# Performance work log

Measured on AMD Instinct MI355X. Metric: run time of the kernel, lower is better.

Reference implementation:

```python
import jax, jax.numpy as jnp
import numpy as np

B, C, H, W = 4, 128, 64, 64

def _conv1x1(x, w, b):
    # 1x1 conv == per-pixel GEMM: [B,C,H,W] x [O,C] -> [B,O,H,W]
    return jnp.einsum('bchw,oc->bohw', x, w) + b[None, :, None, None]

def setup_inputs() -> dict:
    key = jax.random.key(0)
    ks = jax.random.split(key, 11)
    s = 0.02
    return {
        'x0': jax.random.normal(ks[0], (B, C, H, W), jnp.float32),
        'x1': jax.random.normal(ks[1], (B, C, H, W), jnp.float32),
        'g_w': jax.random.normal(ks[2], (C, C), jnp.float32) * s,
        'g_b': jax.random.normal(ks[3], (C,), jnp.float32) * s,
        'theta_w': jax.random.normal(ks[4], (C, C), jnp.float32) * s,
        'theta_b': jax.random.normal(ks[5], (C,), jnp.float32) * s,
        'phi_w': jax.random.normal(ks[6], (C, C), jnp.float32) * s,
        'phi_b': jax.random.normal(ks[7], (C,), jnp.float32) * s,
        'W_w': jax.random.normal(ks[8], (C, C), jnp.float32) * s,
        'W_b': jax.random.normal(ks[9], (C,), jnp.float32) * s,
    }

def reference(x0, x1, g_w, g_b, theta_w, theta_b, phi_w, phi_b, W_w, W_b):
    b, c, h, w = x0.shape
    # g, phi from x0; theta from x1 (cross-attention style)
    g_x = _conv1x1(x0, g_w, g_b).reshape(b, c, -1)          # [B,C,N]
    theta_x = _conv1x1(x1, theta_w, theta_b).reshape(b, c, -1)  # [B,C,N]
    phi_x = _conv1x1(x0, phi_w, phi_b).reshape(b, c, -1)    # [B,C,N]
    # unscaled single-head attention over N=H*W spatial positions
    f = jnp.einsum('bcn,bcm->bnm', theta_x, phi_x)          # [B,N,N]
    attn = jax.nn.softmax(f, axis=-1)
    y = jnp.einsum('bnm,bcm->bcn', attn, g_x)               # [B,C,N]
    y = y.reshape(b, c, h, w)
    return _conv1x1(y, W_w, W_b)
```

## Files before the change

### kernel.cpp

```cpp
#include <hip/hip_runtime.h>
#include <hip/hip_bf16.h>
#include <stdint.h>

#define BB 4
#define CC 128
#define NN 4096
#define NSEG 6
#define KVBLK 32

#define LOG2E 1.4426950408889634f

typedef __bf16 bf16_t;
typedef bf16_t bf16x8 __attribute__((ext_vector_type(8)));
typedef float f32x4 __attribute__((ext_vector_type(4)));
typedef float f32x16 __attribute__((ext_vector_type(16)));
typedef int v2i __attribute__((ext_vector_type(2)));
typedef unsigned int u32;
typedef unsigned short u16;

#if __has_builtin(__builtin_amdgcn_exp2f)
#define EXP2(x) __builtin_amdgcn_exp2f(x)
#else
#define EXP2(x) exp2f(x)
#endif

__device__ __forceinline__ u16 f2bf(float f) {
  union { float f; u32 u; } v; v.f = f;
  u32 r = v.u + 0x7FFFu + ((v.u >> 16) & 1u);
  return (u16)(r >> 16);
}
__device__ __forceinline__ float bf2f(u16 x) {
  union { u32 u; float f; } v; v.u = ((u32)x) << 16; return v.f;
}

__device__ __forceinline__ bf16x8 ldfrag(const u16* p) {
  return *reinterpret_cast<const bf16x8*>(p);
}

__device__ __forceinline__ f32x4 mfma16(bf16x8 a, bf16x8 b, f32x4 c) {
  return __builtin_amdgcn_mfma_f32_16x16x32_bf16(a, b, c, 0, 0, 0);
}
__device__ __forceinline__ f32x16 mfma32(bf16x8 a, bf16x8 b, f32x16 c) {
  return __builtin_amdgcn_mfma_f32_32x32x16_bf16(a, b, c, 0, 0, 0);
}
__device__ __forceinline__ u32 cvtpk(float lo, float hi) {
  u32 d; asm("v_cvt_pk_bf16_f32 %0, %1, %2" : "=v"(d) : "v"(lo), "v"(hi)); return d;
}

__device__ __forceinline__ void async_cp16(const void* g, void* l) {
  __builtin_amdgcn_global_load_lds(
      (const __attribute__((address_space(1))) void*)g,
      (__attribute__((address_space(3))) void*)l, 16, 0, 0);
}

__global__ __launch_bounds__(256) void proj_kernel(
    const float* __restrict__ x0, const float* __restrict__ x1,
    const float* __restrict__ g_w, const float* __restrict__ g_b,
    const float* __restrict__ th_w, const float* __restrict__ th_b,
    const float* __restrict__ ph_w, const float* __restrict__ ph_b,
    u16* __restrict__ qws, u16* __restrict__ kws, u16* __restrict__ vws)
{
  const int t = threadIdx.x;
  const int nt0 = blockIdx.x * 64;
  const int b = blockIdx.y;
  const int p = blockIdx.z;

  __shared__ __align__(16) u16 W_lds[128][136];
  __shared__ __align__(16) u16 xT_lds[64][136];

  const float* x    = (p == 0) ? x1 : x0;
  const float* w    = (p == 0) ? th_w : (p == 1) ? ph_w : g_w;
  const float* bias = (p == 0) ? th_b : (p == 1) ? ph_b : g_b;

  for (int i = 0; i < 16; ++i) {
    int s = t + i * 256;
    int row = s >> 5, c4 = s & 31;
    float4 v = *reinterpret_cast<const float4*>(w + row * 128 + c4 * 4);
    u32 lo = (u32)f2bf(v.x) | ((u32)f2bf(v.y) << 16);
    u32 hi = (u32)f2bf(v.z) | ((u32)f2bf(v.w) << 16);
    *reinterpret_cast<uint2*>(&W_lds[row][c4 * 4]) = make_uint2(lo, hi);
  }
  for (int i = 0; i < 8; ++i) {
    int s = t + i * 256;
    int cp = s >> 4;
    int nc = s & 15;
    float4 v = *reinterpret_cast<const float4*>(x + ((size_t)b * CC + cp) * NN + nt0 + nc * 4);
    xT_lds[nc * 4 + 0][cp] = f2bf(v.x);
    xT_lds[nc * 4 + 1][cp] = f2bf(v.y);
    xT_lds[nc * 4 + 2][cp] = f2bf(v.z);
    xT_lds[nc * 4 + 3][cp] = f2bf(v.w);
  }
  __syncthreads();

  const int w_id = t >> 6, l = t & 63;
  const int lr = l & 15, lh = l >> 4;

  if (p < 2) {
    const float osc = (p == 0) ? LOG2E : 1.0f;
    f32x4 acc[8];
#pragma unroll
    for (int ct = 0; ct < 8; ++ct) acc[ct] = (f32x4){0.f, 0.f, 0.f, 0.f};
#pragma unroll
    for (int kc = 0; kc < 4; ++kc) {
      bf16x8 a = ldfrag(&xT_lds[w_id * 16 + lr][kc * 32 + lh * 8]);
#pragma unroll
      for (int ct = 0; ct < 8; ++ct) {
        bf16x8 bf = ldfrag(&W_lds[ct * 16 + lr][kc * 32 + lh * 8]);
        acc[ct] = mfma16(a, bf, acc[ct]);
      }
    }
    u16* outp = (p == 0) ? qws : kws;
#pragma unroll
    for (int ct = 0; ct < 8; ++ct) {
      float bv = bias[ct * 16 + lr];
#pragma unroll
      for (int r = 0; r < 4; ++r) {
        int n = nt0 + w_id * 16 + lh * 4 + r;
        outp[((size_t)b * NN + n) * CC + ct * 16 + lr] = f2bf((acc[ct][r] + bv) * osc);
      }
    }
  } else {
    f32x4 acc[2][4];
#pragma unroll
    for (int rt = 0; rt < 2; ++rt)
#pragma unroll
      for (int nt = 0; nt < 4; ++nt) acc[rt][nt] = (f32x4){0.f, 0.f, 0.f, 0.f};
#pragma unroll
    for (int kc = 0; kc < 4; ++kc) {
      bf16x8 a0 = ldfrag(&W_lds[w_id * 32 + lr][kc * 32 + lh * 8]);
      bf16x8 a1 = ldfrag(&W_lds[w_id * 32 + 16 + lr][kc * 32 + lh * 8]);
#pragma unroll
      for (int nt = 0; nt < 4; ++nt) {
        bf16x8 bf = ldfrag(&xT_lds[nt * 16 + lr][kc * 32 + lh * 8]);
        acc[0][nt] = mfma16(a0, bf, acc[0][nt]);
        acc[1][nt] = mfma16(a1, bf, acc[1][nt]);
      }
    }
#pragma unroll
    for (int rt = 0; rt < 2; ++rt)
#pragma unroll
      for (int r = 0; r < 4; ++r) {
        int c = w_id * 32 + rt * 16 + lh * 4 + r;
        float bv = bias[c];
#pragma unroll
        for (int nt = 0; nt < 4; ++nt) {
          vws[((size_t)b * CC + c) * NN + nt0 + nt * 16 + lr] = f2bf(acc[rt][nt][r] + bv);
        }
      }
  }
}

__global__ __launch_bounds__(256, 3) void attn_kernel(
    const u16* __restrict__ qws, const u16* __restrict__ kws,
    const u16* __restrict__ vws, u16* __restrict__ yacc,
    float* __restrict__ ml)
{
  const int t = threadIdx.x, wv = t >> 6, l = t & 63;
  const int l31 = l & 31, hi = l >> 5;
  const int q0 = blockIdx.x * 128;
  const int b = blockIdx.y, seg = blockIdx.z;
  const int grp = b * NSEG + seg;
  const int ch0 = (seg < 2) ? seg * 22 : 44 + (seg - 2) * 21;
  const int nch = (seg < 2) ? 22 : 21;
  const int m_base = ch0 * KVBLK;

  __shared__ __align__(16) u16 smem[4 * 4096];
  char* sb = (char*)smem;

  bf16x8 qf[8];
  {
    const u16* qp = qws + ((size_t)b * NN + q0 + wv * 32 + l31) * CC + hi * 8;
#pragma unroll
    for (int kc = 0; kc < 8; ++kc) qf[kc] = *reinterpret_cast<const bf16x8*>(qp + kc * 16);
  }

  const u32 koff = ((u32)(l & 31)) * 256 + ((u32)(wv * 2 + (l >> 5))) * 16;
  const u32 voff = ((u32)((wv & 1) * 64 + l)) * 8192 + ((u32)(wv >> 1)) * 16;
  const char* kgb = (const char*)(kws + ((size_t)b * NN + m_base) * CC);
  const char* vgb = (const char*)(vws + (size_t)b * CC * NN) + (size_t)m_base * 2;

#define ISSUE_K(CH, BOFF) do {                                                       \
    async_cp16(kgb + (size_t)(CH) * 8192 + koff,       sb + (BOFF) + wv * 1024);     \
    async_cp16(kgb + (size_t)(CH) * 8192 + koff + 128, sb + (BOFF) + wv * 1024 + 4096); \
  } while (0)
#define ISSUE_V(CH, BOFF) do {                                                       \
    async_cp16(vgb + (size_t)(CH) * 64 + voff,      sb + (BOFF) + wv * 1024);        \
    async_cp16(vgb + (size_t)(CH) * 64 + voff + 32, sb + (BOFF) + wv * 1024 + 4096); \
  } while (0)
#define SCHED0() __builtin_amdgcn_sched_barrier(0)
#define BAR() do { SCHED0(); __builtin_amdgcn_s_barrier(); SCHED0(); } while (0)

  f32x16 yt[4];
#pragma unroll
  for (int ct = 0; ct < 4; ++ct)
#pragma unroll
    for (int r = 0; r < 16; ++r) yt[ct][r] = 0.f;
  float l_run = 0.f;
  f32x16 stA, stB;
  bf16x8 pbA, pbB;

#define QK_BLOCK(KBASE) do {                                                     \
    const u16* kb = (const u16*)(sb + (KBASE)) + hi * 256 + l31 * 8;             \
    _Pragma("unroll")                                                            \
    for (int r = 0; r < 16; ++r) { stA[r] = 0.f; stB[r] = 0.f; }                 \
    _Pragma("unroll")                                                            \
    for (int kc = 0; kc < 4; ++kc) {                                             \
      stA = mfma32(ldfrag(kb + kc * 512),       qf[kc],     stA);                \
      stB = mfma32(ldfrag(kb + (kc + 4) * 512), qf[kc + 4], stB);                \
    }                                                                            \
  } while (0)

#define PV_BLOCK(VBASE) do {                                                     \
    const u16* vb = (const u16*)(sb + (VBASE)) + hi * 1024 + l31 * 8;            \
    _Pragma("unroll")                                                            \
    for (int ct = 0; ct < 4; ++ct)                                               \
      yt[ct] = mfma32(ldfrag(vb + ct * 256), pbA, yt[ct]);                       \
    _Pragma("unroll")                                                            \
    for (int ct = 0; ct < 4; ++ct)                                               \
      yt[ct] = mfma32(ldfrag(vb + 2048 + ct * 256), pbB, yt[ct]);                \
  } while (0)

#define PACK8(SS, OFF, DEST) do {                                                \
    u32 X0 = cvtpk(SS[(OFF) + 0], SS[(OFF) + 1]);                                \
    u32 X1 = cvtpk(SS[(OFF) + 2], SS[(OFF) + 3]);                                \
    u32 X4 = cvtpk(SS[(OFF) + 4], SS[(OFF) + 5]);                                \
    u32 X5 = cvtpk(SS[(OFF) + 6], SS[(OFF) + 7]);                                \
    v2i s1 = __builtin_amdgcn_permlane32_swap((int)X0, (int)X4, false, false);   \
    v2i s2 = __builtin_amdgcn_permlane32_swap((int)X1, (int)X5, false, false);   \
    int4 bw = make_int4(s1.x, s2.x, s1.y, s2.y);                                 \
    DEST = *reinterpret_cast<bf16x8*>(&bw);                                      \
  } while (0)

#define SM_CONVERT() do {                                                        \
    _Pragma("unroll")                                                            \
    for (int r = 0; r < 16; ++r) stA[r] = EXP2(stA[r] + stB[r]);                 \
    PACK8(stA, 0, pbA);                                                          \
    PACK8(stA, 8, pbB);                                                          \
    _Pragma("unroll")                                                            \
    for (int i2 = 0; i2 < 8; ++i2) stA[i2] = stA[i2] + stA[i2 + 8];              \
    _Pragma("unroll")                                                            \
    for (int i2 = 0; i2 < 4; ++i2) stA[i2] = stA[i2] + stA[i2 + 4];              \
    float ps = (stA[0] + stA[1]) + (stA[2] + stA[3]);                            \
    ps += __shfl_xor(ps, 32);                                                    \
    l_run += ps;                                                                 \
  } while (0)

  ISSUE_K(0, 0);
  ISSUE_K(1, 8192);
  ISSUE_V(0, 16384);
  asm volatile("s_waitcnt vmcnt(4)" ::: "memory");
  BAR();
  QK_BLOCK(0);
  SM_CONVERT();
  asm volatile("s_waitcnt vmcnt(0)" ::: "memory");
  BAR();
  ISSUE_K(2, 0);
  ISSUE_V(1, 24576);

  for (int ch = 1; ch < nch; ++ch) {
    const u32 bK  = (u32)(ch & 1) * 8192;
    const u32 bVp = 16384 + (u32)((ch - 1) & 1) * 8192;
    __builtin_amdgcn_s_setprio(1);
    QK_BLOCK(bK);
    PV_BLOCK(bVp);
    __builtin_amdgcn_s_setprio(0);
    SM_CONVERT();
    asm volatile("s_waitcnt vmcnt(0)" ::: "memory");
    BAR();
    if (ch + 2 < nch) ISSUE_K(ch + 2, bK);
    if (ch + 1 < nch) ISSUE_V(ch + 1, bVp);
  }
  __builtin_amdgcn_s_setprio(1);
  PV_BLOCK(16384 + (u32)((nch - 1) & 1) * 8192);
  __builtin_amdgcn_s_setprio(0);

#undef QK_BLOCK
#undef PV_BLOCK
#undef PACK8
#undef SM_CONVERT
#undef ISSUE_K
#undef ISSUE_V

  __syncthreads();
  const float inv_l = 1.0f / l_run;
  if (l < 32) {
    const size_t row_g = (size_t)grp * NN + q0 + wv * 32 + l31;
    ml[row_g] = l_run;
  }
  u16* yp_base = yacc + ((size_t)grp * NN + q0 + wv * 32) * CC;
#pragma unroll
  for (int half = 0; half < 2; ++half) {
    if ((wv >> 1) == half) {
      u16* eps = smem + (wv & 1) * 4352;
#pragma unroll
      for (int ct = 0; ct < 4; ++ct)
#pragma unroll
        for (int g = 0; g < 4; ++g) {
          u32 w0 = cvtpk(yt[ct][4 * g + 0] * inv_l, yt[ct][4 * g + 1] * inv_l);
          u32 w1 = cvtpk(yt[ct][4 * g + 2] * inv_l, yt[ct][4 * g + 3] * inv_l);
          *reinterpret_cast<uint2*>(&eps[l31 * 136 + ct * 32 + g * 8 + hi * 4]) = make_uint2(w0, w1);
        }
#pragma unroll
      for (int pass = 0; pass < 8; ++pass) {
        int q_r = pass * 4 + (l >> 4);
        int cchunk = (l & 15) * 8;
        uint4 v = *reinterpret_cast<const uint4*>(&eps[q_r * 136 + cchunk]);
        *reinterpret_cast<uint4*>(yp_base + (size_t)q_r * CC + cchunk) = v;
      }
    }
    __syncthreads();
  }
}

__global__ __launch_bounds__(256) void outproj_kernel(
    const u16* __restrict__ yacc, const float* __restrict__ ml,
    const float* __restrict__ Ww, const float* __restrict__ Wb,
    float* __restrict__ out)
{
  const int t = threadIdx.x;
  const int nt0 = blockIdx.x * 64;
  const int b = blockIdx.y;

  __shared__ __align__(16) u16 W_lds[128][136];
  __shared__ __align__(16) u16 y_lds[64][136];

  for (int i = 0; i < 16; ++i) {
    int s = t + i * 256;
    int row = s >> 5, c4 = s & 31;
    float4 v = *reinterpret_cast<const float4*>(Ww + row * 128 + c4 * 4);
    u32 lo = (u32)f2bf(v.x) | ((u32)f2bf(v.y) << 16);
    u32 hi = (u32)f2bf(v.z) | ((u32)f2bf(v.w) << 16);
    *reinterpret_cast<uint2*>(&W_lds[row][c4 * 4]) = make_uint2(lo, hi);
  }
#pragma unroll
  for (int pass = 0; pass < 4; ++pass) {
    int row = pass * 16 + (t >> 4);
    int li = t & 15;
    int n = nt0 + row;
    float l_s[NSEG];
    float Wsum = 0.f;
#pragma unroll
    for (int s = 0; s < NSEG; ++s) {
      l_s[s] = ml[(size_t)(b * NSEG + s) * NN + n];
      Wsum += l_s[s];
    }
    float inv = 1.0f / Wsum;
    float o[8];
#pragma unroll
    for (int j = 0; j < 8; ++j) o[j] = 0.f;
#pragma unroll
    for (int s = 0; s < NSEG; ++s) {
      uint4 v = *reinterpret_cast<const uint4*>(
          yacc + ((size_t)(b * NSEG + s) * NN + n) * CC + li * 8);
      const u16* h = reinterpret_cast<const u16*>(&v);
      float w = l_s[s];
#pragma unroll
      for (int j = 0; j < 8; ++j) o[j] += w * bf2f(h[j]);
    }
    u32 p0 = (u32)f2bf(o[0] * inv) | ((u32)f2bf(o[1] * inv) << 16);
    u32 p1 = (u32)f2bf(o[2] * inv) | ((u32)f2bf(o[3] * inv) << 16);
    u32 p2 = (u32)f2bf(o[4] * inv) | ((u32)f2bf(o[5] * inv) << 16);
    u32 p3 = (u32)f2bf(o[6] * inv) | ((u32)f2bf(o[7] * inv) << 16);
    *reinterpret_cast<uint4*>(&y_lds[row][li * 8]) = make_uint4(p0, p1, p2, p3);
  }
  __syncthreads();

  const int w_id = t >> 6, l = t & 63;
  const int lr = l & 15, lh = l >> 4;

  f32x4 acc[2][4];
#pragma unroll
  for (int rt = 0; rt < 2; ++rt)
#pragma unroll
    for (int nt = 0; nt < 4; ++nt) acc[rt][nt] = (f32x4){0.f, 0.f, 0.f, 0.f};
#pragma unroll
  for (int kc = 0; kc < 4; ++kc) {
    bf16x8 a0 = ldfrag(&W_lds[w_id * 32 + lr][kc * 32 + lh * 8]);
    bf16x8 a1 = ldfrag(&W_lds[w_id * 32 + 16 + lr][kc * 32 + lh * 8]);
#pragma unroll
    for (int nt = 0; nt < 4; ++nt) {
      bf16x8 bf = ldfrag(&y_lds[nt * 16 + lr][kc * 32 + lh * 8]);
      acc[0][nt] = mfma16(a0, bf, acc[0][nt]);
      acc[1][nt] = mfma16(a1, bf, acc[1][nt]);
    }
  }
#pragma unroll
  for (int rt = 0; rt < 2; ++rt)
#pragma unroll
    for (int r = 0; r < 4; ++r) {
      int c = w_id * 32 + rt * 16 + lh * 4 + r;
      float bv = Wb[c];
#pragma unroll
      for (int nt = 0; nt < 4; ++nt)
        out[((size_t)b * CC + c) * NN + nt0 + nt * 16 + lr] = acc[rt][nt][r] + bv;
    }
}

extern "C" void kernel_launch(void* const* d_in, const int* in_sizes, int n_in,
                              void* d_out, int out_size, void* d_ws, size_t ws_size,
                              hipStream_t stream) {
  const float* x0   = (const float*)d_in[0];
  const float* x1   = (const float*)d_in[1];
  const float* g_w  = (const float*)d_in[2];
  const float* g_b  = (const float*)d_in[3];
  const float* th_w = (const float*)d_in[4];
  const float* th_b = (const float*)d_in[5];
  const float* ph_w = (const float*)d_in[6];
  const float* ph_b = (const float*)d_in[7];
  const float* Ww   = (const float*)d_in[8];
  const float* Wb   = (const float*)d_in[9];

  char* ws = (char*)d_ws;
  u16* qws    = (u16*)(ws + 0);
  u16* kws    = (u16*)(ws + (size_t)4194304);
  u16* vws    = (u16*)(ws + (size_t)8388608);
  float* mlp  = (float*)(ws + (size_t)12582912);
  u16* yacc   = (u16*)(ws + (size_t)13631488);

  dim3 gp(64, 4, 3);
  proj_kernel<<<gp, 256, 0, stream>>>(x0, x1, g_w, g_b, th_w, th_b, ph_w, ph_b,
                                      qws, kws, vws);
  dim3 ga(32, 4, NSEG);
  attn_kernel<<<ga, 256, 0, stream>>>(qws, kws, vws, yacc, mlp);
  dim3 go(64, 4);
  outproj_kernel<<<go, 256, 0, stream>>>(yacc, mlp, Ww, Wb, (float*)d_out);
}
```

Before: 65.27 us.

## Retile attention to 16x16 MFMA with 64-query blocks and four KV segments

The attention kernel moves from 32x32x16 MFMA tiles over 32 queries per wave to 16x16x32 MFMA tiles over 16 queries per wave, so each block now covers 64 queries. The probability tile is staged through a small per-wave LDS buffer instead of being rearranged with permlane swaps. The KV split drops from six uneven segments to four equal ones, the grid grows along the query axis, and the occupancy hint rises to 4 blocks per CU. The goal is more, lighter blocks and fewer partial results to merge, at the cost of reloading each K/V tile for fewer queries and using the smaller MFMA shape.

```diff
diff --git a/kernel.cpp b/kernel.cpp
--- a/kernel.cpp
+++ b/kernel.cpp
@@ -5,16 +5,17 @@
 #define BB 4
 #define CC 128
 #define NN 4096
-#define NSEG 6
+#define NSEG 4
+#define SEGLEN (NN / NSEG)
 #define KVBLK 32
+#define NCH (SEGLEN / KVBLK)
 
 #define LOG2E 1.4426950408889634f
+#define PPITCH 40
 
 typedef __bf16 bf16_t;
 typedef bf16_t bf16x8 __attribute__((ext_vector_type(8)));
 typedef float f32x4 __attribute__((ext_vector_type(4)));
-typedef float f32x16 __attribute__((ext_vector_type(16)));
-typedef int v2i __attribute__((ext_vector_type(2)));
 typedef unsigned int u32;
 typedef unsigned short u16;
 
@@ -39,9 +40,6 @@
 
 __device__ __forceinline__ f32x4 mfma16(bf16x8 a, bf16x8 b, f32x4 c) {
   return __builtin_amdgcn_mfma_f32_16x16x32_bf16(a, b, c, 0, 0, 0);
-}
-__device__ __forceinline__ f32x16 mfma32(bf16x8 a, bf16x8 b, f32x16 c) {
-  return __builtin_amdgcn_mfma_f32_32x32x16_bf16(a, b, c, 0, 0, 0);
 }
 __device__ __forceinline__ u32 cvtpk(float lo, float hi) {
   u32 d; asm("v_cvt_pk_bf16_f32 %0, %1, %2" : "=v"(d) : "v"(lo), "v"(hi)); return d;
@@ -150,28 +148,27 @@
   }
 }
 
-__global__ __launch_bounds__(256, 3) void attn_kernel(
+__global__ __launch_bounds__(256, 4) void attn_kernel(
     const u16* __restrict__ qws, const u16* __restrict__ kws,
     const u16* __restrict__ vws, u16* __restrict__ yacc,
     float* __restrict__ ml)
 {
   const int t = threadIdx.x, wv = t >> 6, l = t & 63;
-  const int l31 = l & 31, hi = l >> 5;
-  const int q0 = blockIdx.x * 128;
+  const int q16 = l & 15, g = l >> 4;
+  const int q0 = blockIdx.x * 64;
   const int b = blockIdx.y, seg = blockIdx.z;
   const int grp = b * NSEG + seg;
-  const int ch0 = (seg < 2) ? seg * 22 : 44 + (seg - 2) * 21;
-  const int nch = (seg < 2) ? 22 : 21;
-  const int m_base = ch0 * KVBLK;
-
-  __shared__ __align__(16) u16 smem[4 * 4096];
+  const int m_base = seg * SEGLEN;
+
+  __shared__ __align__(16) u16 smem[16384 + 4 * 16 * PPITCH];
   char* sb = (char*)smem;
-
-  bf16x8 qf[8];
+  u16* Pw = smem + 16384 + wv * (16 * PPITCH);
+
+  bf16x8 qf[4];
   {
-    const u16* qp = qws + ((size_t)b * NN + q0 + wv * 32 + l31) * CC + hi * 8;
-#pragma unroll
-    for (int kc = 0; kc < 8; ++kc) qf[kc] = *reinterpret_cast<const bf16x8*>(qp + kc * 16);
+    const u16* qp = qws + ((size_t)b * NN + q0 + wv * 16 + q16) * CC + g * 8;
+#pragma unroll
+    for (int kc = 0; kc < 4; ++kc) qf[kc] = *reinterpret_cast<const bf16x8*>(qp + kc * 32);
   }
 
   const u32 koff = ((u32)(l & 31)) * 256 + ((u32)(wv * 2 + (l >> 5))) * 16;
@@ -190,57 +187,41 @@
 #define SCHED0() __builtin_amdgcn_sched_barrier(0)
 #define BAR() do { SCHED0(); __builtin_amdgcn_s_barrier(); SCHED0(); } while (0)
 
-  f32x16 yt[4];
-#pragma unroll
-  for (int ct = 0; ct < 4; ++ct)
-#pragma unroll
-    for (int r = 0; r < 16; ++r) yt[ct][r] = 0.f;
+  f32x4 yt[8];
+#pragma unroll
+  for (int ct = 0; ct < 8; ++ct) yt[ct] = (f32x4){0.f, 0.f, 0.f, 0.f};
   float l_run = 0.f;
-  f32x16 stA, stB;
-  bf16x8 pbA, pbB;
+  f32x4 st0, st1;
 
 #define QK_BLOCK(KBASE) do {                                                     \
-    const u16* kb = (const u16*)(sb + (KBASE)) + hi * 256 + l31 * 8;             \
-    _Pragma("unroll")                                                            \
-    for (int r = 0; r < 16; ++r) { stA[r] = 0.f; stB[r] = 0.f; }                 \
+    const u16* kb = (const u16*)(sb + (KBASE)) + (g * 32 + q16) * 8;             \
+    st0 = (f32x4){0.f, 0.f, 0.f, 0.f};                                           \
+    st1 = (f32x4){0.f, 0.f, 0.f, 0.f};                                           \
     _Pragma("unroll")                                                            \
     for (int kc = 0; kc < 4; ++kc) {                                             \
-      stA = mfma32(ldfrag(kb + kc * 512),       qf[kc],     stA);                \
-      stB = mfma32(ldfrag(kb + (kc + 4) * 512), qf[kc + 4], stB);                \
+      st0 = mfma16(ldfrag(kb + kc * 1024),       qf[kc], st0);                   \
+      st1 = mfma16(ldfrag(kb + kc * 1024 + 128), qf[kc], st1);                   \
     }                                                                            \
   } while (0)
 
 #define PV_BLOCK(VBASE) do {                                                     \
-    const u16* vb = (const u16*)(sb + (VBASE)) + hi * 1024 + l31 * 8;            \
+    bf16x8 pb = ldfrag(Pw + q16 * PPITCH + g * 8);                               \
+    const u16* vb = (const u16*)(sb + (VBASE)) + (g * 128 + q16) * 8;            \
     _Pragma("unroll")                                                            \
-    for (int ct = 0; ct < 4; ++ct)                                               \
-      yt[ct] = mfma32(ldfrag(vb + ct * 256), pbA, yt[ct]);                       \
-    _Pragma("unroll")                                                            \
-    for (int ct = 0; ct < 4; ++ct)                                               \
-      yt[ct] = mfma32(ldfrag(vb + 2048 + ct * 256), pbB, yt[ct]);                \
-  } while (0)
-
-#define PACK8(SS, OFF, DEST) do {                                                \
-    u32 X0 = cvtpk(SS[(OFF) + 0], SS[(OFF) + 1]);                                \
-    u32 X1 = cvtpk(SS[(OFF) + 2], SS[(OFF) + 3]);                                \
-    u32 X4 = cvtpk(SS[(OFF) + 4], SS[(OFF) + 5]);                                \
-    u32 X5 = cvtpk(SS[(OFF) + 6], SS[(OFF) + 7]);                                \
-    v2i s1 = __builtin_amdgcn_permlane32_swap((int)X0, (int)X4, false, false);   \
-    v2i s2 = __builtin_amdgcn_permlane32_swap((int)X1, (int)X5, false, false);   \
-    int4 bw = make_int4(s1.x, s2.x, s1.y, s2.y);                                 \
-    DEST = *reinterpret_cast<bf16x8*>(&bw);                                      \
+    for (int ct = 0; ct < 8; ++ct)                                               \
+      yt[ct] = mfma16(ldfrag(vb + ct * 128), pb, yt[ct]);                        \
   } while (0)
 
 #define SM_CONVERT() do {                                                        \
     _Pragma("unroll")                                                            \
-    for (int r = 0; r < 16; ++r) stA[r] = EXP2(stA[r] + stB[r]);                 \
-    PACK8(stA, 0, pbA);                                                          \
-    PACK8(stA, 8, pbB);                                                          \
-    _Pragma("unroll")                                                            \
-    for (int i2 = 0; i2 < 8; ++i2) stA[i2] = stA[i2] + stA[i2 + 8];              \
-    _Pragma("unroll")                                                            \
-    for (int i2 = 0; i2 < 4; ++i2) stA[i2] = stA[i2] + stA[i2 + 4];              \
-    float ps = (stA[0] + stA[1]) + (stA[2] + stA[3]);                            \
+    for (int r = 0; r < 4; ++r) { st0[r] = EXP2(st0[r]); st1[r] = EXP2(st1[r]); } \
+    u32 X0 = cvtpk(st0[0], st0[1]), X1 = cvtpk(st0[2], st0[3]);                  \
+    u32 X2 = cvtpk(st1[0], st1[1]), X3 = cvtpk(st1[2], st1[3]);                  \
+    *reinterpret_cast<uint2*>(Pw + q16 * PPITCH + g * 4)      = make_uint2(X0, X1); \
+    *reinterpret_cast<uint2*>(Pw + q16 * PPITCH + 16 + g * 4) = make_uint2(X2, X3); \
+    float ps = ((st0[0] + st0[1]) + (st0[2] + st0[3]))                           \
+             + ((st1[0] + st1[1]) + (st1[2] + st1[3]));                          \
+    ps += __shfl_xor(ps, 16);                                                    \
     ps += __shfl_xor(ps, 32);                                                    \
     l_run += ps;                                                                 \
   } while (0)
@@ -257,7 +238,7 @@
   ISSUE_K(2, 0);
   ISSUE_V(1, 24576);
 
-  for (int ch = 1; ch < nch; ++ch) {
+  for (int ch = 1; ch < NCH; ++ch) {
     const u32 bK  = (u32)(ch & 1) * 8192;
     const u32 bVp = 16384 + (u32)((ch - 1) & 1) * 8192;
     __builtin_amdgcn_s_setprio(1);
@@ -267,48 +248,40 @@
     SM_CONVERT();
     asm volatile("s_waitcnt vmcnt(0)" ::: "memory");
     BAR();
-    if (ch + 2 < nch) ISSUE_K(ch + 2, bK);
-    if (ch + 1 < nch) ISSUE_V(ch + 1, bVp);
+    if (ch + 2 < NCH) ISSUE_K(ch + 2, bK);
+    if (ch + 1 < NCH) ISSUE_V(ch + 1, bVp);
   }
   __builtin_amdgcn_s_setprio(1);
-  PV_BLOCK(16384 + (u32)((nch - 1) & 1) * 8192);
+  PV_BLOCK(16384 + (u32)((NCH - 1) & 1) * 8192);
   __builtin_amdgcn_s_setprio(0);
 
 #undef QK_BLOCK
 #undef PV_BLOCK
-#undef PACK8
 #undef SM_CONVERT
 #undef ISSUE_K
 #undef ISSUE_V
 
   __syncthreads();
   const float inv_l = 1.0f / l_run;
-  if (l < 32) {
-    const size_t row_g = (size_t)grp * NN + q0 + wv * 32 + l31;
-    ml[row_g] = l_run;
-  }
-  u16* yp_base = yacc + ((size_t)grp * NN + q0 + wv * 32) * CC;
-#pragma unroll
-  for (int half = 0; half < 2; ++half) {
-    if ((wv >> 1) == half) {
-      u16* eps = smem + (wv & 1) * 4352;
-#pragma unroll
-      for (int ct = 0; ct < 4; ++ct)
-#pragma unroll
-        for (int g = 0; g < 4; ++g) {
-          u32 w0 = cvtpk(yt[ct][4 * g + 0] * inv_l, yt[ct][4 * g + 1] * inv_l);
-          u32 w1 = cvtpk(yt[ct][4 * g + 2] * inv_l, yt[ct][4 * g + 3] * inv_l);
-          *reinterpret_cast<uint2*>(&eps[l31 * 136 + ct * 32 + g * 8 + hi * 4]) = make_uint2(w0, w1);
-        }
-#pragma unroll
-      for (int pass = 0; pass < 8; ++pass) {
-        int q_r = pass * 4 + (l >> 4);
-        int cchunk = (l & 15) * 8;
-        uint4 v = *reinterpret_cast<const uint4*>(&eps[q_r * 136 + cchunk]);
-        *reinterpret_cast<uint4*>(yp_base + (size_t)q_r * CC + cchunk) = v;
-      }
-    }
-    __syncthreads();
+  if (l < 16) {
+    ml[(size_t)grp * NN + q0 + wv * 16 + l] = l_run;
+  }
+  u16* yp_base = yacc + ((size_t)grp * NN + q0 + wv * 16) * CC;
+  {
+    u16* eps = smem + wv * 2176;
+#pragma unroll
+    for (int ct = 0; ct < 8; ++ct) {
+      u32 w0 = cvtpk(yt[ct][0] * inv_l, yt[ct][1] * inv_l);
+      u32 w1 = cvtpk(yt[ct][2] * inv_l, yt[ct][3] * inv_l);
+      *reinterpret_cast<uint2*>(&eps[q16 * 136 + ct * 16 + g * 4]) = make_uint2(w0, w1);
+    }
+#pragma unroll
+    for (int pass = 0; pass < 4; ++pass) {
+      int q_r = pass * 4 + g;
+      int cchunk = q16 * 8;
+      uint4 v = *reinterpret_cast<const uint4*>(&eps[q_r * 136 + cchunk]);
+      *reinterpret_cast<uint4*>(yp_base + (size_t)q_r * CC + cchunk) = v;
+    }
   }
 }
 
@@ -420,7 +393,7 @@
   dim3 gp(64, 4, 3);
   proj_kernel<<<gp, 256, 0, stream>>>(x0, x1, g_w, g_b, th_w, th_b, ph_w, ph_b,
                                       qws, kws, vws);
-  dim3 ga(32, 4, NSEG);
+  dim3 ga(64, 4, NSEG);
   attn_kernel<<<ga, 256, 0, stream>>>(qws, kws, vws, yacc, mlp);
   dim3 go(64, 4);
   outproj_kernel<<<go, 256, 0, stream>>>(yacc, mlp, Ww, Wb, (float*)d_out);
```

New measurement: 87.35 us. 1.34x slower.
